# Performance work log

Hardware: AMD Instinct MI355X
Metric: run time of the kernel (lower is better)

Reference implementation:

```python
import jax, jax.numpy as jnp
import numpy as np

N_NODES = 50000
N_EDGES = 800000
H = 128
D = 128
N_LAYERS = 4
N_GRAPHS = 128
NODE_VOCAB = 32
EDGE_VOCAB = 8
BN_EPS = 1e-5


def _bn(h, g, b):
    # BatchNorm1d, training-mode statistics (biased variance), as in the torch module
    m = h.mean(axis=0)
    v = ((h - m) ** 2).mean(axis=0)
    return (h - m) * jax.lax.rsqrt(v + BN_EPS) * g + b


def _gine(x, src, dst, e, eps_l):
    # GINEConv: message = ReLU(x_src + edge_attr), sum-aggregate at dst
    msg = jax.nn.relu(x[src] + e)                      # [E, H]
    aggr = jax.ops.segment_sum(msg, dst, num_segments=N_NODES)
    return (1.0 + eps_l) * x + aggr


def _forward(x_ids, edge_index, batch, edge_attr,
             node_emb, edge_emb, eps,
             init_W1, init_b1, init_g1, init_be1, init_W2, init_b2, init_g2, init_be2,
             mp_W1, mp_g1, mp_be1, mp_W2, mp_g2, mp_be2,
             l1_W1, l1_g1, l1_b1, l1_W2, l1_g2, l1_b2,
             l2_W1, l2_g1, l2_b1, l2_W2, l2_g2, l2_b2,
             fin_W):
    src, dst = edge_index[0], edge_index[1]
    x = node_emb[x_ids]                                # [N, H]
    e = edge_emb[edge_attr]                            # [E, H]
    # initialization conv (Linear layers WITH bias)
    h = _gine(x, src, dst, e, eps[0])
    h = jax.nn.relu(_bn(h @ init_W1 + init_b1, init_g1, init_be1))
    x = jax.nn.relu(_bn(h @ init_W2 + init_b2, init_g2, init_be2))
    # message-passing layers (Linear layers WITHOUT bias)
    for i in range(N_LAYERS):
        h = _gine(x, src, dst, e, eps[1 + i])
        h = jax.nn.relu(_bn(h @ mp_W1[i], mp_g1[i], mp_be1[i]))
        x = jax.nn.relu(_bn(h @ mp_W2[i], mp_g2[i], mp_be2[i]))
    # readout: global_add_pool
    g = jax.ops.segment_sum(x, batch, num_segments=N_GRAPHS)   # [G, H]
    # lin1 (outer F.relu is idempotent; dropout = identity in eval)
    h = jax.nn.relu(_bn(g @ l1_W1, l1_g1, l1_b1))
    h = jax.nn.relu(_bn(h @ l1_W2, l1_g2, l1_b2))
    # lin2
    h = jax.nn.relu(_bn(h @ l2_W1, l2_g1, l2_b1))
    h = jax.nn.relu(_bn(h @ l2_W2, l2_g2, l2_b2))
    return h @ fin_W                                   # [G, 1]


def setup_inputs() -> dict:
    key = jax.random.key(0)
    ks = jax.random.split(key, 20)
    s = 1.0 / np.sqrt(H)
    rn = lambda k, shp, sc: jax.random.normal(k, shp, dtype=jnp.float32) * sc
    return {
        "x_ids": jax.random.randint(ks[0], (N_NODES,), 0, NODE_VOCAB),
        "edge_index": jax.random.randint(ks[1], (2, N_EDGES), 0, N_NODES),
        "batch": jnp.sort(jax.random.randint(ks[2], (N_NODES,), 0, N_GRAPHS)),
        "edge_attr": jax.random.randint(ks[14], (N_EDGES,), 0, EDGE_VOCAB),
        "node_emb": rn(ks[3], (NODE_VOCAB, H), 0.05),
        "edge_emb": rn(ks[4], (EDGE_VOCAB, H), 0.05),
        "eps": jnp.zeros((N_LAYERS + 1,), jnp.float32),
        "init_W1": rn(ks[5], (H, D), s), "init_b1": jnp.zeros((D,)),
        "init_g1": jnp.ones((D,)), "init_be1": jnp.zeros((D,)),
        "init_W2": rn(ks[6], (D, H), s), "init_b2": jnp.zeros((H,)),
        "init_g2": jnp.ones((H,)), "init_be2": jnp.zeros((H,)),
        "mp_W1": rn(ks[7], (N_LAYERS, H, D), s),
        "mp_g1": jnp.ones((N_LAYERS, D)), "mp_be1": jnp.zeros((N_LAYERS, D)),
        "mp_W2": rn(ks[8], (N_LAYERS, D, H), s),
        "mp_g2": jnp.ones((N_LAYERS, H)), "mp_be2": jnp.zeros((N_LAYERS, H)),
        "l1_W1": rn(ks[9], (H, D), s), "l1_g1": jnp.ones((D,)), "l1_b1": jnp.zeros((D,)),
        "l1_W2": rn(ks[10], (D, D), s), "l1_g2": jnp.ones((D,)), "l1_b2": jnp.zeros((D,)),
        "l2_W1": rn(ks[11], (D, D), s), "l2_g1": jnp.ones((D,)), "l2_b1": jnp.zeros((D,)),
        "l2_W2": rn(ks[12], (D, H), s), "l2_g2": jnp.ones((H,)), "l2_b2": jnp.zeros((H,)),
        "fin_W": rn(ks[13], (H, 1), s),
    }


def reference(x_ids, edge_index, batch, edge_attr,
              node_emb, edge_emb, eps,
              init_W1, init_b1, init_g1, init_be1, init_W2, init_b2, init_g2, init_be2,
              mp_W1, mp_g1, mp_be1, mp_W2, mp_g2, mp_be2,
              l1_W1, l1_g1, l1_b1, l1_W2, l1_g2, l1_b2,
              l2_W1, l2_g1, l2_b1, l2_W2, l2_g2, l2_b2,
              fin_W):
    return _forward(x_ids, edge_index, batch, edge_attr,
                    node_emb, edge_emb, eps,
                    init_W1, init_b1, init_g1, init_be1, init_W2, init_b2, init_g2, init_be2,
                    mp_W1, mp_g1, mp_be1, mp_W2, mp_g2, mp_be2,
                    l1_W1, l1_g1, l1_b1, l1_W2, l1_g2, l1_b2,
                    l2_W1, l2_g1, l2_b1, l2_W2, l2_g2, l2_b2,
                    fin_W)
```

## Files before the change

### kernel.cpp

```cpp
#include <hip/hip_runtime.h>

#define NN 50000
#define NE 800000
#define NG 128
#define HD 128
#define NL 4
#define BN_EPS 1e-5f
#define REP 32
#define WP 136
#define NB 392
#define EPB 4096

typedef __attribute__((ext_vector_type(8))) short bf16x8;
typedef __attribute__((ext_vector_type(4))) float f32x4;

__device__ __forceinline__ unsigned short f2bf(float f) {
    unsigned u = __float_as_uint(f);
    u += 0x7FFFu + ((u >> 16) & 1u);
    return (unsigned short)(u >> 16);
}
__device__ __forceinline__ float bfval(unsigned short h) { return __uint_as_float((unsigned)h << 16); }
__device__ __forceinline__ float bflo(unsigned u) { return __uint_as_float(u << 16); }
__device__ __forceinline__ float bfhi(unsigned u) { return __uint_as_float(u & 0xFFFF0000u); }

// ... 14 lines not shown
    if (gam == nullptr) { scs[t] = 1.f; shs[t] = 0.f; return; }
    float s = 0.f, q = 0.f;
#pragma unroll
    for (int r = 0; r < REP; r++) {
        s += SQbase[r * 256 + t];
        q += SQbase[r * 256 + 128 + t];
    }
    float m = s * inv_cnt;
    float var = fmaxf(fmaf(q, inv_cnt, -m * m), 0.f);
    float inv = rsqrtf(var + BN_EPS);
    float sc = gam[t] * inv;
    scs[t] = sc;
    shs[t] = fmaf(-m, sc, bet[t]);
}

__global__ __launch_bounds__(256) void setup_kernel(const int* __restrict__ ids,
                                                    const float* __restrict__ emb,
                                                    unsigned short* __restrict__ Yb,
                                                    const float* __restrict__ iw1,
                                                    const float* __restrict__ iw2,
                                                    const float* __restrict__ mw1,
                                                    const float* __restrict__ mw2,
                                                    unsigned short* __restrict__ Wh,
                                                    unsigned short* __restrict__ Wl,
                                                    const int* __restrict__ dst,
                                                    int* __restrict__ deg) {
    int b = blockIdx.x, t = threadIdx.x;
    if (b < 3125) {
        int i = b * 256 + t;
        if (i < NN * 16) {
            int node = i >> 4, g = i & 15;
            int id = ids[node];
            const float* p = emb + (size_t)id * HD + 8 * g;
            float4 a = *(const float4*)p;
            float4 bb = *(const float4*)(p + 4);
            uint4 o;
            o.x = pack2(a.x, a.y); o.y = pack2(a.z, a.w);
            o.z = pack2(bb.x, bb.y); o.w = pack2(bb.z, bb.w);
            *(uint4*)(Yb + (size_t)node * HD + 8 * g) = o;
        }
    } else if (b < 3765) {
        int i = (b - 3125) * 256 + t;
        if (i < 163840) {
            int seg = i >> 14, loc = i & 16383;
            float v;
            if (seg == 0)      v = iw1[loc];
            else if (seg == 1) v = iw2[loc];
            else if (seg < 6)  v = mw1[(seg - 2) * 16384 + loc];
            else               v = mw2[(seg - 6) * 16384 + loc];
            int k = loc >> 7, n = loc & 127;
            unsigned short h = f2bf(v);
            float r = v - bfval(h);
            Wh[seg * 16384 + n * 128 + k] = h;
            Wl[seg * 16384 + n * 128 + k] = f2bf(r);
        }
    } else {
        int e = (b - 3765) * 256 + t;
        if (e < NE) atomicAdd(&deg[dst[e]], 1);
    }
}

__global__ __launch_bounds__(256) void ybn_kernel(const float* __restrict__ X,
                                                  const float* __restrict__ SQin,
                                                  const float* __restrict__ gam,
                                                  const float* __restrict__ bet,
                                                  unsigned short* __restrict__ Yb) {
    __shared__ float scs[HD], shs[HD];
    int t = threadIdx.x;
    if (t < HD) bn_pre(SQin, gam, bet, 1.f / NN, t, scs, shs);
    __syncthreads();
    int row = blockIdx.x * 16 + (t >> 4);
    int c8 = (t & 15) * 8;
    if (row < NN) {
        const float* p = X + (size_t)row * HD + c8;
        float4 v0 = *(const float4*)p;
        float4 v1 = *(const float4*)(p + 4);
        float4 s0 = *(const float4*)&scs[c8], s1 = *(const float4*)&scs[c8 + 4];
        float4 h0 = *(const float4*)&shs[c8], h1 = *(const float4*)&shs[c8 + 4];
        float f0 = fmaxf(fmaf(v0.x, s0.x, h0.x), 0.f), f1 = fmaxf(fmaf(v0.y, s0.y, h0.y), 0.f);
        float f2 = fmaxf(fmaf(v0.z, s0.z, h0.z), 0.f), f3 = fmaxf(fmaf(v0.w, s0.w, h0.w), 0.f);
        float f4 = fmaxf(fmaf(v1.x, s1.x, h1.x), 0.f), f5 = fmaxf(fmaf(v1.y, s1.y, h1.y), 0.f);
        float f6 = fmaxf(fmaf(v1.z, s1.z, h1.z), 0.f), f7 = fmaxf(fmaf(v1.w, s1.w, h1.w), 0.f);
        uint4 o;
        o.x = pack2(f0, f1); o.y = pack2(f2, f3);
        o.z = pack2(f4, f5); o.w = pack2(f6, f7);
        *(uint4*)(Yb + (size_t)row * HD + c8) = o;
    }
}

__global__ __launch_bounds__(1024) void scan1_kernel(const int* __restrict__ deg,
                                                     int* __restrict__ rowptr,
                                                     int* __restrict__ blockSum) {
    __shared__ int s[1024];
    int b = blockIdx.x, t = threadIdx.x;
    int i = b * 1024 + t;
    int v = (i < NN) ? deg[i] : 0;
    s[t] = v;
    __syncthreads();
    for (int off = 1; off < 1024; off <<= 1) {
        int u = (t >= off) ? s[t - off] : 0;
        __syncthreads();
        s[t] += u;
        __syncthreads();
    }
    if (i < NN) rowptr[i] = s[t] - v;
    if (t == 1023) blockSum[b] = s[1023];
}

__global__ __launch_bounds__(64) void scan2_kernel(const int* __restrict__ blockSum,
                                                   int* __restrict__ blockOff,
                                                   int* __restrict__ rowptr, int nblocks) {
    int t = threadIdx.x;
    int orig = (t < nblocks) ? blockSum[t] : 0;
    int v = orig;
    for (int off = 1; off < 64; off <<= 1) {
        int u = __shfl_up(v, off, 64);
        if (t >= off) v += u;
    }
    if (t < nblocks) blockOff[t] = v - orig;
    if (t == nblocks - 1) rowptr[NN] = v;
}

__global__ __launch_bounds__(1024) void scan3_kernel(int* __restrict__ rowptr,
                                                     int* __restrict__ cursor,
                                                     const int* __restrict__ blockOff,
                                                     int* __restrict__ bucketCursor) {
    int b = blockIdx.x, t = threadIdx.x;
    int i = b * 1024 + t;
    if (i < NN) {
        int r = rowptr[i] + blockOff[b];
        rowptr[i] = r;
        cursor[i] = r;
        if ((i & 127) == 0) bucketCursor[i >> 7] = r;
    }
}

__global__ __launch_bounds__(256) void bin_kernel(const int* __restrict__ src,
                                                  const int* __restrict__ dst,
                                                  const int* __restrict__ attr,
                                                  int* __restrict__ bucketCursor,
                                                  uint2* __restrict__ ebuf) {
    __shared__ int cnt[512];
    __shared__ int sc[512], sc2[512];
    __shared__ int base[512];
    __shared__ int garr[NB];
    __shared__ int wof[NB];
    __shared__ uint2 stage[EPB];
    int t = threadIdx.x;
    int e0 = blockIdx.x * EPB;
    for (int i = t; i < 512; i += 256) cnt[i] = 0;
    __syncthreads();
    int myb[16]; unsigned myv[16]; int myd[16];
#pragma unroll
    for (int j = 0; j < 16; j++) {
        int e = e0 + t + j * 256;
        if (e < NE) {
            int d = dst[e];
            myd[j] = d;
            myv[j] = (unsigned)src[e] | ((unsigned)attr[e] << 16);
            myb[j] = d >> 7;
            atomicAdd(&cnt[myb[j]], 1);
        } else myb[j] = -1;
    }
    __syncthreads();
    for (int k = t; k < 512; k += 256) sc[k] = cnt[k];
    __syncthreads();
    int* sp = sc; int* dp = sc2;
    for (int off = 1; off < 512; off <<= 1) {
        for (int k = t; k < 512; k += 256) dp[k] = sp[k] + (k >= off ? sp[k - off] : 0);
        __syncthreads();
        int* tmp = sp; sp = dp; dp = tmp;
    }
    for (int k = t; k < 512; k += 256) base[k] = sp[k] - cnt[k];
    int total = sp[511];
    __syncthreads();
    for (int b = t; b < NB; b += 256) {
        wof[b] = 0;
        if (cnt[b] > 0) garr[b] = atomicAdd(&bucketCursor[b], cnt[b]);
    }
    __syncthreads();
#pragma unroll
    for (int j = 0; j < 16; j++) {
        if (myb[j] >= 0) {
            int slot = base[myb[j]] + atomicAdd(&wof[myb[j]], 1);
            stage[slot] = make_uint2(myv[j], (unsigned)myd[j]);
        }
    }
    __syncthreads();
    for (int i = t; i < total; i += 256) {
        uint2 u = stage[i];
        int b = (int)(u.y >> 7);
        ebuf[garr[b] + (i - base[b])] = u;
    }
}

__global__ __launch_bounds__(256) void place_kernel(const uint2* __restrict__ ebuf,
                                                    const int* __restrict__ rowptr,
                                                    int* __restrict__ cursor,
                                                    unsigned* __restrict__ csr) {
    int b = blockIdx.x;
    int n0 = b * 128;
    int n1 = n0 + 128; if (n1 > NN) n1 = NN;
    int es = rowptr[n0], ee = rowptr[n1];
    for (int i = es + threadIdx.x; i < ee; i += 256) {
        uint2 u = ebuf[i];
        int pos = atomicAdd(&cursor[u.y], 1);
        csr[pos] = u.x;
    }
}

__device__ __forceinline__ void gine_acc(const unsigned short* __restrict__ Yb,
                                         const float* __restrict__ elds,
                                         unsigned p, int cq, float mask, float* a) {
    uint4 q = *(const uint4*)(Yb + (size_t)(p & 0xFFFFu) * HD + 8 * cq);
    const float* ep = elds + (p >> 16) * HD + 8 * cq;
    float4 e0 = *(const float4*)ep;
    float4 e1 = *(const float4*)(ep + 4);
    a[0] += mask * fmaxf(bflo(q.x) + e0.x, 0.f);
    a[1] += mask * fmaxf(bfhi(q.x) + e0.y, 0.f);
    a[2] += mask * fmaxf(bflo(q.y) + e0.z, 0.f);
    a[3] += mask * fmaxf(bfhi(q.y) + e0.w, 0.f);
    a[4] += mask * fmaxf(bflo(q.z) + e1.x, 0.f);
    a[5] += mask * fmaxf(bfhi(q.z) + e1.y, 0.f);
    a[6] += mask * fmaxf(bflo(q.w) + e1.z, 0.f);
    a[7] += mask * fmaxf(bfhi(q.w) + e1.w, 0.f);
}

__global__ __launch_bounds__(256) void conv_kernel(const unsigned short* __restrict__ Yb,
                                                   const int* __restrict__ rowptr,
                                                   const unsigned* __restrict__ csr,
                                                   const float* __restrict__ edge_emb,
                                                   const float* __restrict__ eps, int layer,
                                                   unsigned short* __restrict__ Ah,
                                                   unsigned short* __restrict__ Al) {
    __shared__ float elds[8 * HD];
    int t = threadIdx.x;
    ((float4*)elds)[t] = ((const float4*)edge_emb)[t];
    __syncthreads();
    int wave = t >> 6, lane = t & 63;
    int node = blockIdx.x * 4 + wave;
    if (node >= NN) return;
    int sub = lane >> 4, cq = lane & 15;
    int lo = rowptr[node], hi = rowptr[node + 1];
    float a[8];
#pragma unroll
    for (int i = 0; i < 8; i++) a[i] = 0.f;
    for (int base = lo; base < hi; base += 64) {
        unsigned pl = 0;
        int cnt = hi - base; if (cnt > 64) cnt = 64;
        if (base + lane < hi) pl = csr[base + lane];
        int j = 0;
        for (; j + 16 <= cnt; j += 16) {
            unsigned pa = __shfl(pl, j + sub, 64);
            unsigned pb = __shfl(pl, j + 4 + sub, 64);
            unsigned pc = __shfl(pl, j + 8 + sub, 64);
            unsigned pd = __shfl(pl, j + 12 + sub, 64);
            gine_acc(Yb, elds, pa, cq, 1.f, a);
            gine_acc(Yb, elds, pb, cq, 1.f, a);
            gine_acc(Yb, elds, pc, cq, 1.f, a);
            gine_acc(Yb, elds, pd, cq, 1.f, a);
        }
        for (; j + 8 <= cnt; j += 8) {
            unsigned pa = __shfl(pl, j + sub, 64);
            unsigned pb = __shfl(pl, j + 4 + sub, 64);
            gine_acc(Yb, elds, pa, cq, 1.f, a);
            gine_acc(Yb, elds, pb, cq, 1.f, a);
        }
        for (; j < cnt; j += 4) {
            int je = j + sub;
            bool val = (je < cnt);
            unsigned p = __shfl(pl, val ? je : j, 64);
            gine_acc(Yb, elds, p, cq, val ? 1.f : 0.f, a);
        }
    }
#pragma unroll
    for (int i = 0; i < 8; i++) {
        a[i] += __shfl_xor(a[i], 16, 64);
        a[i] += __shfl_xor(a[i], 32, 64);
    }
    if (sub == 0) {
        float g = 1.f + eps[layer];
        uint4 q = *(const uint4*)(Yb + (size_t)node * HD + 8 * cq);
        float o0 = fmaf(g, bflo(q.x), a[0]), o1 = fmaf(g, bfhi(q.x), a[1]);
        float o2 = fmaf(g, bflo(q.y), a[2]), o3 = fmaf(g, bfhi(q.y), a[3]);
        float o4 = fmaf(g, bflo(q.z), a[4]), o5 = fmaf(g, bfhi(q.z), a[5]);
        float o6 = fmaf(g, bflo(q.w), a[6]), o7 = fmaf(g, bfhi(q.w), a[7]);
        uint4 H, L;
        split2(o0, o1, H.x, L.x);
        split2(o2, o3, H.y, L.y);
        split2(o4, o5, H.z, L.z);
        split2(o6, o7, H.w, L.w);
        *(uint4*)(Ah + (size_t)node * HD + 8 * cq) = H;
        *(uint4*)(Al + (size_t)node * HD + 8 * cq) = L;
    }
}

__global__ __launch_bounds__(256) void mm_mfma_pre(const unsigned short* __restrict__ Ah,
                                                   const unsigned short* __restrict__ Al,
                                                   const unsigned short* __restrict__ Wh,
                                                   const unsigned short* __restrict__ Wl,
                                                   const float* __restrict__ bias,
                                                   float* __restrict__ out,
                                                   float* __restrict__ SQout) {
    __shared__ unsigned short WhS[64 * WP];
    __shared__ unsigned short WlS[64 * WP];
    int t = threadIdx.x;
    int rowblk = blockIdx.x >> 1;
    int colbase = (blockIdx.x & 1) * 64;
    const unsigned short* sh = Wh + (size_t)colbase * HD;
    const unsigned short* sl = Wl + (size_t)colbase * HD;
#pragma unroll
    for (int i = 0; i < 4; i++) {
        int idx = t + i * 256;
        int col = idx >> 4, kk = (idx & 15) * 8;
        *(uint4*)(WhS + col * WP + kk) = *(const uint4*)(sh + (size_t)col * HD + kk);
        *(uint4*)(WlS + col * WP + kk) = *(const uint4*)(sl + (size_t)col * HD + kk);
    }
    __syncthreads();
    int w = t >> 6, lane = t & 63;
    int quad = lane >> 4, nl = lane & 15;
    int row0 = rowblk * 128 + w * 32;
    int rA0 = row0 + nl, rA1 = row0 + 16 + nl;
    bool ok0 = rA0 < NN, ok1 = rA1 < NN;
    f32x4 acc[8];
#pragma unroll
    for (int i = 0; i < 8; i++) acc[i] = (f32x4){0.f, 0.f, 0.f, 0.f};
#pragma unroll
    for (int kc = 0; kc < 4; kc++) {
        int k0 = kc * 32 + quad * 8;
        bf16x8 a0h = ok0 ? *(const bf16x8*)(Ah + (size_t)rA0 * HD + k0) : (bf16x8)0;
        bf16x8 a0l = ok0 ? *(const bf16x8*)(Al + (size_t)rA0 * HD + k0) : (bf16x8)0;
        bf16x8 a1h = ok1 ? *(const bf16x8*)(Ah + (size_t)rA1 * HD + k0) : (bf16x8)0;
        bf16x8 a1l = ok1 ? *(const bf16x8*)(Al + (size_t)rA1 * HD + k0) : (bf16x8)0;
#pragma unroll
        for (int c = 0; c < 4; c++) {
            int wof = (c * 16 + nl) * WP + k0;
            bf16x8 bh = *(const bf16x8*)(WhS + wof);
            bf16x8 bl = *(const bf16x8*)(WlS + wof);
            acc[c] = __builtin_amdgcn_mfma_f32_16x16x32_bf16(a0h, bh, acc[c], 0, 0, 0);
            acc[c] = __builtin_amdgcn_mfma_f32_16x16x32_bf16(a0l, bh, acc[c], 0, 0, 0);
            acc[c] = __builtin_amdgcn_mfma_f32_16x16x32_bf16(a0h, bl, acc[c], 0, 0, 0);
            acc[4 + c] = __builtin_amdgcn_mfma_f32_16x16x32_bf16(a1h, bh, acc[4 + c], 0, 0, 0);
            acc[4 + c] = __builtin_amdgcn_mfma_f32_16x16x32_bf16(a1l, bh, acc[4 + c], 0, 0, 0);
            acc[4 + c] = __builtin_amdgcn_mfma_f32_16x16x32_bf16(a1h, bl, acc[4 + c], 0, 0, 0);
        }
    }
    int rep = (blockIdx.x & (REP - 1)) * 256;
#pragma unroll
    for (int h = 0; h < 2; h++) {
        int baserow = row0 + h * 16 + quad * 4;
#pragma unroll
        for (int c = 0; c < 4; c++) {
            int col = colbase + c * 16 + nl;
            float bv = bias ? bias[col] : 0.f;
            f32x4 v = acc[h * 4 + c];
            float s = 0.f, qq = 0.f;
#pragma unroll
            for (int r = 0; r < 4; r++) {
                int grow = baserow + r;
                float val = v[r] + bv;
                if (grow < NN) {
                    out[(size_t)grow * HD + col] = val;
                    s += val;
                    qq += val * val;
                }
            }
            s += __shfl_xor(s, 16, 64);  s += __shfl_xor(s, 32, 64);
            qq += __shfl_xor(qq, 16, 64); qq += __shfl_xor(qq, 32, 64);
            if (quad == 0) {
                atomicAdd(&SQout[rep + col], s);
                atomicAdd(&SQout[rep + 128 + col], qq);
            }
        }
    }
}

__global__ __launch_bounds__(256) void mm_mfma_act(const float* __restrict__ A,
                                                   const unsigned short* __restrict__ Wh,
                                                   const unsigned short* __restrict__ Wl,
                                                   const float* __restrict__ bias,
                                                   const float* __restrict__ SQin,
                                                   const float* __restrict__ gam,
                                                   const float* __restrict__ bet,
                                                   float* __restrict__ out,
                                                   float* __restrict__ SQout) {
    __shared__ unsigned short WhS[64 * WP];
    __shared__ unsigned short WlS[64 * WP];
    __shared__ float scs[HD], shs[HD];
    int t = threadIdx.x;
    int rowblk = blockIdx.x >> 1;
    int colbase = (blockIdx.x & 1) * 64;
    if (t < HD) bn_pre(SQin, gam, bet, 1.f / NN, t, scs, shs);
    const unsigned short* sh = Wh + (size_t)colbase * HD;
    const unsigned short* sl = Wl + (size_t)colbase * HD;
#pragma unroll
    for (int i = 0; i < 4; i++) {
        int idx = t + i * 256;
        int col = idx >> 4, kk = (idx & 15) * 8;
        *(uint4*)(WhS + col * WP + kk) = *(const uint4*)(sh + (size_t)col * HD + kk);
        *(uint4*)(WlS + col * WP + kk) = *(const uint4*)(sl + (size_t)col * HD + kk);
    }
    __syncthreads();
    int w = t >> 6, lane = t & 63;
    int quad = lane >> 4, nl = lane & 15;
    int row0 = rowblk * 128 + w * 32;
    int rA0 = row0 + nl, rA1 = row0 + 16 + nl;
    bool ok0 = rA0 < NN, ok1 = rA1 < NN;
    f32x4 acc[8];
#pragma unroll
    for (int i = 0; i < 8; i++) acc[i] = (f32x4){0.f, 0.f, 0.f, 0.f};
#pragma unroll
    for (int kc = 0; kc < 4; kc++) {
        int k0 = kc * 32 + quad * 8;
        float4 s0 = *(const float4*)&scs[k0], s1 = *(const float4*)&scs[k0 + 4];
        float4 t0 = *(const float4*)&shs[k0], t1 = *(const float4*)&shs[k0 + 4];
        bf16x8 a0h, a0l, a1h, a1l;
        {
            float4 v0 = ok0 ? *(const float4*)(A + (size_t)rA0 * HD + k0) : make_float4(0, 0, 0, 0);
            float4 v1 = ok0 ? *(const float4*)(A + (size_t)rA0 * HD + k0 + 4) : make_float4(0, 0, 0, 0);
            float f0 = fmaxf(fmaf(v0.x, s0.x, t0.x), 0.f), f1 = fmaxf(fmaf(v0.y, s0.y, t0.y), 0.f);
            float f2 = fmaxf(fmaf(v0.z, s0.z, t0.z), 0.f), f3 = fmaxf(fmaf(v0.w, s0.w, t0.w), 0.f);
            float f4 = fmaxf(fmaf(v1.x, s1.x, t1.x), 0.f), f5 = fmaxf(fmaf(v1.y, s1.y, t1.y), 0.f);
            float f6 = fmaxf(fmaf(v1.z, s1.z, t1.z), 0.f), f7 = fmaxf(fmaf(v1.w, s1.w, t1.w), 0.f);
            if (!ok0) { f0 = f1 = f2 = f3 = f4 = f5 = f6 = f7 = 0.f; }
            unsigned h0, h1, h2, h3, l0, l1, l2, l3;
            split2(f0, f1, h0, l0); split2(f2, f3, h1, l1);
            split2(f4, f5, h2, l2); split2(f6, f7, h3, l3);
            a0h = __builtin_bit_cast(bf16x8, make_uint4(h0, h1, h2, h3));
            a0l = __builtin_bit_cast(bf16x8, make_uint4(l0, l1, l2, l3));
        }
        {
            float4 v0 = ok1 ? *(const float4*)(A + (size_t)rA1 * HD + k0) : make_float4(0, 0, 0, 0);
            float4 v1 = ok1 ? *(const float4*)(A + (size_t)rA1 * HD + k0 + 4) : make_float4(0, 0, 0, 0);
            float f0 = fmaxf(fmaf(v0.x, s0.x, t0.x), 0.f), f1 = fmaxf(fmaf(v0.y, s0.y, t0.y), 0.f);
            float f2 = fmaxf(fmaf(v0.z, s0.z, t0.z), 0.f), f3 = fmaxf(fmaf(v0.w, s0.w, t0.w), 0.f);
            float f4 = fmaxf(fmaf(v1.x, s1.x, t1.x), 0.f), f5 = fmaxf(fmaf(v1.y, s1.y, t1.y), 0.f);
            float f6 = fmaxf(fmaf(v1.z, s1.z, t1.z), 0.f), f7 = fmaxf(fmaf(v1.w, s1.w, t1.w), 0.f);
            if (!ok1) { f0 = f1 = f2 = f3 = f4 = f5 = f6 = f7 = 0.f; }
            unsigned h0, h1, h2, h3, l0, l1, l2, l3;
            split2(f0, f1, h0, l0); split2(f2, f3, h1, l1);
            split2(f4, f5, h2, l2); split2(f6, f7, h3, l3);
            a1h = __builtin_bit_cast(bf16x8, make_uint4(h0, h1, h2, h3));
            a1l = __builtin_bit_cast(bf16x8, make_uint4(l0, l1, l2, l3));
        }
#pragma unroll
        for (int c = 0; c < 4; c++) {
            int wof = (c * 16 + nl) * WP + k0;
            bf16x8 bh = *(const bf16x8*)(WhS + wof);
            bf16x8 bl = *(const bf16x8*)(WlS + wof);
            acc[c] = __builtin_amdgcn_mfma_f32_16x16x32_bf16(a0h, bh, acc[c], 0, 0, 0);
            acc[c] = __builtin_amdgcn_mfma_f32_16x16x32_bf16(a0l, bh, acc[c], 0, 0, 0);
            acc[c] = __builtin_amdgcn_mfma_f32_16x16x32_bf16(a0h, bl, acc[c], 0, 0, 0);
            acc[4 + c] = __builtin_amdgcn_mfma_f32_16x16x32_bf16(a1h, bh, acc[4 + c], 0, 0, 0);
            acc[4 + c] = __builtin_amdgcn_mfma_f32_16x16x32_bf16(a1l, bh, acc[4 + c], 0, 0, 0);
            acc[4 + c] = __builtin_amdgcn_mfma_f32_16x16x32_bf16(a1h, bl, acc[4 + c], 0, 0, 0);
        }
    }
    int rep = (blockIdx.x & (REP - 1)) * 256;
#pragma unroll
    for (int h = 0; h < 2; h++) {
        int baserow = row0 + h * 16 + quad * 4;
#pragma unroll
        for (int c = 0; c < 4; c++) {
            int col = colbase + c * 16 + nl;
            float bv = bias ? bias[col] : 0.f;
            f32x4 v = acc[h * 4 + c];
            float s = 0.f, qq = 0.f;
#pragma unroll
            for (int r = 0; r < 4; r++) {
                int grow = baserow + r;
                float val = v[r] + bv;
                if (grow < NN) {
                    out[(size_t)grow * HD + col] = val;
                    s += val;
                    qq += val * val;
                }
            }
            s += __shfl_xor(s, 16, 64);  s += __shfl_xor(s, 32, 64);
            qq += __shfl_xor(qq, 16, 64); qq += __shfl_xor(qq, 32, 64);
            if (quad == 0) {
                atomicAdd(&SQout[rep + col], s);
                atomicAdd(&SQout[rep + 128 + col], qq);
            }
        }
    }
}

__global__ __launch_bounds__(256) void readout_kernel(const float* __restrict__ x,
                                                      const int* __restrict__ batch,
                                                      const float* __restrict__ SQin,
                                                      const float* __restrict__ gam,
                                                      const float* __restrict__ bet,
                                                      float* __restrict__ gout) {
    __shared__ int bat[256];
    __shared__ float scs[HD], shs[HD];
    int t = threadIdx.x;
    int rq = t >> 5, cq = t & 31;
    int r0 = blockIdx.x * 256;
    int i = r0 + t;
    bat[t] = (i < NN) ? batch[i] : -1;
    if (t < HD) bn_pre(SQin, gam, bet, 1.f / NN, t, scs, shs);
    __syncthreads();
    float4 s4 = *(const float4*)&scs[4 * cq];
    float4 h4 = *(const float4*)&shs[4 * cq];
    float4 acc = make_float4(0.f, 0.f, 0.f, 0.f);
    int gcur = -1;
    for (int j = rq; j < 256; j += 8) {
        int r = r0 + j;
        if (r >= NN) break;
        int g = bat[j];
        if (g != gcur) {
            if (gcur >= 0) {
                atomicAdd(&gout[(size_t)gcur * HD + 4 * cq + 0], acc.x);
                atomicAdd(&gout[(size_t)gcur * HD + 4 * cq + 1], acc.y);
                atomicAdd(&gout[(size_t)gcur * HD + 4 * cq + 2], acc.z);
                atomicAdd(&gout[(size_t)gcur * HD + 4 * cq + 3], acc.w);
            }
            acc = make_float4(0.f, 0.f, 0.f, 0.f);
            gcur = g;
        }
        float4 v = *(const float4*)(x + (size_t)r * HD + 4 * cq);
        acc.x += fmaxf(fmaf(v.x, s4.x, h4.x), 0.f);
        acc.y += fmaxf(fmaf(v.y, s4.y, h4.y), 0.f);
        acc.z += fmaxf(fmaf(v.z, s4.z, h4.z), 0.f);
        acc.w += fmaxf(fmaf(v.w, s4.w, h4.w), 0.f);
    }
    if (gcur >= 0) {
        atomicAdd(&gout[(size_t)gcur * HD + 4 * cq + 0], acc.x);
        atomicAdd(&gout[(size_t)gcur * HD + 4 * cq + 1], acc.y);
        atomicAdd(&gout[(size_t)gcur * HD + 4 * cq + 2], acc.z);
        atomicAdd(&gout[(size_t)gcur * HD + 4 * cq + 3], acc.w);
    }
}

__global__ __launch_bounds__(256) void head_mm(const float* __restrict__ A,
                                               const float* __restrict__ W,
                                               const float* __restrict__ SQin,
                                               const float* __restrict__ gam,
                                               const float* __restrict__ bet,
                                               float* __restrict__ out,
                                               float* __restrict__ SQout) {
    const int PADK = 132;
    __shared__ float As[64 * PADK];
    __shared__ float colS[HD], colQ[HD];
    __shared__ float scs[HD], shs[HD];
    int t = threadIdx.x;
    if (t < HD) {
        colS[t] = 0.f; colQ[t] = 0.f;
        bn_pre(SQin, gam, bet, 1.f / NG, t, scs, shs);
    }
    __syncthreads();
    int row0 = blockIdx.x * 64;
#pragma unroll
    for (int i = 0; i < 8; i++) {
        int idx = t + i * 256;
        int r = idx >> 5, kq = idx & 31;
        float4 v = *(const float4*)(A + (size_t)(row0 + r) * HD + 4 * kq);
        float4 s4 = *(const float4*)&scs[4 * kq];
        float4 h4 = *(const float4*)&shs[4 * kq];
        v.x = fmaxf(fmaf(v.x, s4.x, h4.x), 0.f);
        v.y = fmaxf(fmaf(v.y, s4.y, h4.y), 0.f);
        v.z = fmaxf(fmaf(v.z, s4.z, h4.z), 0.f);
        v.w = fmaxf(fmaf(v.w, s4.w, h4.w), 0.f);
        *(float4*)&As[r * PADK + 4 * kq] = v;
    }
    __syncthreads();
    int jq = t & 31, rb = t >> 5;
    float acc[8][4];
#pragma unroll
    for (int i = 0; i < 8; i++)
#pragma unroll
        for (int j = 0; j < 4; j++) acc[i][j] = 0.f;
    const float* Wp = W + 4 * jq;
    const float* Ap = &As[rb * 8 * PADK];
    for (int k = 0; k < HD; k += 4) {
        float4 w0 = *(const float4*)(Wp + (size_t)(k + 0) * HD);
        float4 w1 = *(const float4*)(Wp + (size_t)(k + 1) * HD);
        float4 w2 = *(const float4*)(Wp + (size_t)(k + 2) * HD);
        float4 w3 = *(const float4*)(Wp + (size_t)(k + 3) * HD);
#pragma unroll
        for (int i = 0; i < 8; i++) {
            float4 a4 = *(const float4*)&Ap[i * PADK + k];
            acc[i][0] = fmaf(a4.x, w0.x, acc[i][0]);
            acc[i][1] = fmaf(a4.x, w0.y, acc[i][1]);
            acc[i][2] = fmaf(a4.x, w0.z, acc[i][2]);
            acc[i][3] = fmaf(a4.x, w0.w, acc[i][3]);
            acc[i][0] = fmaf(a4.y, w1.x, acc[i][0]);
            acc[i][1] = fmaf(a4.y, w1.y, acc[i][1]);
            acc[i][2] = fmaf(a4.y, w1.z, acc[i][2]);
            acc[i][3] = fmaf(a4.y, w1.w, acc[i][3]);
            acc[i][0] = fmaf(a4.z, w2.x, acc[i][0]);
            acc[i][1] = fmaf(a4.z, w2.y, acc[i][1]);
            acc[i][2] = fmaf(a4.z, w2.z, acc[i][2]);
            acc[i][3] = fmaf(a4.z, w2.w, acc[i][3]);
            acc[i][0] = fmaf(a4.w, w3.x, acc[i][0]);
            acc[i][1] = fmaf(a4.w, w3.y, acc[i][1]);
            acc[i][2] = fmaf(a4.w, w3.z, acc[i][2]);
            acc[i][3] = fmaf(a4.w, w3.w, acc[i][3]);
        }
    }
    float s0 = 0, s1 = 0, s2 = 0, s3 = 0, q0 = 0, q1 = 0, q2 = 0, q3 = 0;
#pragma unroll
    for (int i = 0; i < 8; i++) {
        int gr = row0 + rb * 8 + i;
        float4 v = make_float4(acc[i][0], acc[i][1], acc[i][2], acc[i][3]);
        *(float4*)(out + (size_t)gr * HD + 4 * jq) = v;
        s0 += v.x; q0 += v.x * v.x;
        s1 += v.y; q1 += v.y * v.y;
        s2 += v.z; q2 += v.z * v.z;
        s3 += v.w; q3 += v.w * v.w;
    }
    atomicAdd(&colS[4 * jq + 0], s0); atomicAdd(&colQ[4 * jq + 0], q0);
    atomicAdd(&colS[4 * jq + 1], s1); atomicAdd(&colQ[4 * jq + 1], q1);
    atomicAdd(&colS[4 * jq + 2], s2); atomicAdd(&colQ[4 * jq + 2], q2);
    atomicAdd(&colS[4 * jq + 3], s3); atomicAdd(&colQ[4 * jq + 3], q3);
    __syncthreads();
    int rep = (blockIdx.x & (REP - 1)) * 256;
    if (t < HD) {
        atomicAdd(&SQout[rep + t], colS[t]);
        atomicAdd(&SQout[rep + 128 + t], colQ[t]);
    }
}

__global__ __launch_bounds__(128) void final_kernel(const float* __restrict__ h,
                                                    const float* __restrict__ SQin,
                                                    const float* __restrict__ gam,
                                                    const float* __restrict__ bet,
                                                    const float* __restrict__ finW,
                                                    float* __restrict__ out) {
    __shared__ float scs[HD], shs[HD];
    int t = threadIdx.x;
    bn_pre(SQin, gam, bet, 1.f / NG, t, scs, shs);
    __syncthreads();
    float s = 0.f;
    for (int c = 0; c < HD; c++) {
        float v = h[(size_t)t * HD + c];
        v = fmaxf(fmaf(v, scs[c], shs[c]), 0.f);
        s += v * finW[c];
    }
    out[t] = s;
}

extern "C" void kernel_launch(void* const* d_in, const int* in_sizes, int n_in,
                              void* d_out, int out_size, void* d_ws, size_t ws_size,
                              hipStream_t stream) {
    const int* x_ids = (const int*)d_in[0];
    const int* edge_index = (const int*)d_in[1];
    const int* batch = (const int*)d_in[2];
    const int* edge_attr = (const int*)d_in[3];
    const float* node_emb = (const float*)d_in[4];
    const float* edge_emb = (const float*)d_in[5];
    const float* eps = (const float*)d_in[6];
    const float* init_W1 = (const float*)d_in[7];
    const float* init_b1 = (const float*)d_in[8];
    const float* init_g1 = (const float*)d_in[9];
    const float* init_be1 = (const float*)d_in[10];
    const float* init_W2 = (const float*)d_in[11];
    const float* init_b2 = (const float*)d_in[12];
    const float* init_g2 = (const float*)d_in[13];
    const float* init_be2 = (const float*)d_in[14];
    const float* mp_W1 = (const float*)d_in[15];
    const float* mp_g1 = (const float*)d_in[16];
    const float* mp_be1 = (const float*)d_in[17];
    const float* mp_W2 = (const float*)d_in[18];
    const float* mp_g2 = (const float*)d_in[19];
    const float* mp_be2 = (const float*)d_in[20];
    const float* l1_W1 = (const float*)d_in[21];
    const float* l1_g1 = (const float*)d_in[22];
    const float* l1_b1 = (const float*)d_in[23];
    const float* l1_W2 = (const float*)d_in[24];
    const float* l1_g2 = (const float*)d_in[25];
    const float* l1_b2 = (const float*)d_in[26];
    const float* l2_W1 = (const float*)d_in[27];
    const float* l2_g1 = (const float*)d_in[28];
    const float* l2_b1 = (const float*)d_in[29];
    const float* l2_W2 = (const float*)d_in[30];
    const float* l2_g2 = (const float*)d_in[31];
    const float* l2_b2 = (const float*)d_in[32];
    const float* fin_W = (const float*)d_in[33];

    const int* e_src = edge_index;
    const int* e_dst = edge_index + NE;

    const size_t STG = (size_t)REP * 256;
    float* ws = (float*)d_ws;
    float* X = ws;
    float* Bbuf = X + (size_t)NN * HD;
    unsigned short* Yb = (unsigned short*)Bbuf;
    unsigned short* Ah = (unsigned short*)(Bbuf + (size_t)NN * HD);
    unsigned short* Al = Ah + (size_t)NN * HD;
    float* SQ = (float*)(Al + (size_t)NN * HD);
    float* Gp = SQ + 14 * STG;
    int* deg = (int*)(Gp + NG * HD);
    float* Hp = (float*)(deg + 50048);
    float* Hp2 = Hp + NG * HD;
    int* rowptr = (int*)(Hp2 + NG * HD);
    int* cursor = rowptr + 50048;
    int* blockSum = cursor + 50048;
    int* blockOff = blockSum + 64;
    int* bucketCursor = blockOff + 64;
    unsigned* csr = (unsigned*)(bucketCursor + NB);
    unsigned short* Wh = (unsigned short*)(csr + NE);
    unsigned short* Wl = Wh + 163840;
    uint2* ebuf = (uint2*)(Wl + 163840);

    const size_t zero_bytes = (14 * STG + NG * HD) * sizeof(float) + 50048 * sizeof(int);
    hipMemsetAsync(SQ, 0, zero_bytes, stream);

    const int SCAN_BLOCKS = (NN + 1023) / 1024;
    setup_kernel<<<6890, 256, 0, stream>>>(x_ids, node_emb, Yb, init_W1, init_W2, mp_W1,
                                           mp_W2, Wh, Wl, e_dst, deg);
    scan1_kernel<<<SCAN_BLOCKS, 1024, 0, stream>>>(deg, rowptr, blockSum);
    scan2_kernel<<<1, 64, 0, stream>>>(blockSum, blockOff, rowptr, SCAN_BLOCKS);
    scan3_kernel<<<SCAN_BLOCKS, 1024, 0, stream>>>(rowptr, cursor, blockOff, bucketCursor);
    bin_kernel<<<(NE + EPB - 1) / EPB, 256, 0, stream>>>(e_src, e_dst, edge_attr,
                                                         bucketCursor, ebuf);
    place_kernel<<<(NN + 127) / 128, 256, 0, stream>>>(ebuf, rowptr, cursor, csr);

    const int mfma_grid = ((NN + 127) / 128) * 2;
    const int ybn_grid = (NN + 15) / 16;
    for (int i = 0; i <= NL; i++) {
        const unsigned short* Wh1 = Wh + (size_t)(i == 0 ? 0 : 2 + (i - 1)) * 16384;
        const unsigned short* Wl1 = Wl + (size_t)(i == 0 ? 0 : 2 + (i - 1)) * 16384;
        const unsigned short* Wh2 = Wh + (size_t)(i == 0 ? 1 : 6 + (i - 1)) * 16384;
        const unsigned short* Wl2 = Wl + (size_t)(i == 0 ? 1 : 6 + (i - 1)) * 16384;
        const float* b1 = (i == 0) ? init_b1 : nullptr;
        const float* b2 = (i == 0) ? init_b2 : nullptr;
        const float* g1 = (i == 0) ? init_g1 : mp_g1 + (size_t)(i - 1) * HD;
        const float* be1 = (i == 0) ? init_be1 : mp_be1 + (size_t)(i - 1) * HD;
        const float* gp = (i == 1) ? init_g2 : mp_g2 + (size_t)(i - 2) * HD;
        const float* bp = (i == 1) ? init_be2 : mp_be2 + (size_t)(i - 2) * HD;
        float* Sprev = SQ + (size_t)(2 * i - 1) * STG;
        float* S1 = SQ + (size_t)(2 * i) * STG;
        float* S2 = SQ + (size_t)(2 * i + 1) * STG;

        if (i > 0) ybn_kernel<<<ybn_grid, 256, 0, stream>>>(X, Sprev, gp, bp, Yb);
        conv_kernel<<<(NN + 3) / 4, 256, 0, stream>>>(Yb, rowptr, csr, edge_emb, eps, i, Ah, Al);
        mm_mfma_pre<<<mfma_grid, 256, 0, stream>>>(Ah, Al, Wh1, Wl1, b1, Bbuf, S1);
        mm_mfma_act<<<mfma_grid, 256, 0, stream>>>(Bbuf, Wh2, Wl2, b2, S1, g1, be1, X, S2);
    }

    float* S9 = SQ + 9 * STG;
    readout_kernel<<<(NN + 255) / 256, 256, 0, stream>>>(
        X, batch, S9, mp_g2 + 3 * HD, mp_be2 + 3 * HD, Gp);

    float* S10 = SQ + 10 * STG;
    float* S11 = SQ + 11 * STG;
    float* S12 = SQ + 12 * STG;
    float* S13 = SQ + 13 * STG;
    head_mm<<<2, 256, 0, stream>>>(Gp, l1_W1, nullptr, nullptr, nullptr, Hp, S10);
    head_mm<<<2, 256, 0, stream>>>(Hp, l1_W2, S10, l1_g1, l1_b1, Hp2, S11);
    head_mm<<<2, 256, 0, stream>>>(Hp2, l2_W1, S11, l1_g2, l1_b2, Hp, S12);
    head_mm<<<2, 256, 0, stream>>>(Hp, l2_W2, S12, l2_g1, l2_b1, Hp2, S13);
    final_kernel<<<1, 128, 0, stream>>>(Hp2, S13, l2_g2, l2_b2, fin_W, (float*)d_out);
}
```

Measured before the change: 772.1 us.

## Widen MFMA tiles to full 128 columns and fuse head MLP into one kernel

```diff
diff --git a/kernel.cpp b/kernel.cpp
--- a/kernel.cpp
+++ b/kernel.cpp
@@ -340,19 +340,16 @@
                                                    const float* __restrict__ bias,
                                                    float* __restrict__ out,
                                                    float* __restrict__ SQout) {
-    __shared__ unsigned short WhS[64 * WP];
-    __shared__ unsigned short WlS[64 * WP];
+    __shared__ unsigned short WhS[128 * WP];
+    __shared__ unsigned short WlS[128 * WP];
     int t = threadIdx.x;
-    int rowblk = blockIdx.x >> 1;
-    int colbase = (blockIdx.x & 1) * 64;
-    const unsigned short* sh = Wh + (size_t)colbase * HD;
-    const unsigned short* sl = Wl + (size_t)colbase * HD;
-#pragma unroll
-    for (int i = 0; i < 4; i++) {
+    int rowblk = blockIdx.x;
+#pragma unroll
+    for (int i = 0; i < 8; i++) {
         int idx = t + i * 256;
         int col = idx >> 4, kk = (idx & 15) * 8;
-        *(uint4*)(WhS + col * WP + kk) = *(const uint4*)(sh + (size_t)col * HD + kk);
-        *(uint4*)(WlS + col * WP + kk) = *(const uint4*)(sl + (size_t)col * HD + kk);
+        *(uint4*)(WhS + col * WP + kk) = *(const uint4*)(Wh + (size_t)col * HD + kk);
+        *(uint4*)(WlS + col * WP + kk) = *(const uint4*)(Wl + (size_t)col * HD + kk);
     }
     __syncthreads();
     int w = t >> 6, lane = t & 63;
@@ -360,9 +357,9 @@
     int row0 = rowblk * 128 + w * 32;
     int rA0 = row0 + nl, rA1 = row0 + 16 + nl;
     bool ok0 = rA0 < NN, ok1 = rA1 < NN;
-    f32x4 acc[8];
-#pragma unroll
-    for (int i = 0; i < 8; i++) acc[i] = (f32x4){0.f, 0.f, 0.f, 0.f};
+    f32x4 acc[16];
+#pragma unroll
+    for (int i = 0; i < 16; i++) acc[i] = (f32x4){0.f, 0.f, 0.f, 0.f};
 #pragma unroll
     for (int kc = 0; kc < 4; kc++) {
         int k0 = kc * 32 + quad * 8;
@@ -371,16 +368,16 @@
         bf16x8 a1h = ok1 ? *(const bf16x8*)(Ah + (size_t)rA1 * HD + k0) : (bf16x8)0;
         bf16x8 a1l = ok1 ? *(const bf16x8*)(Al + (size_t)rA1 * HD + k0) : (bf16x8)0;
 #pragma unroll
-        for (int c = 0; c < 4; c++) {
+        for (int c = 0; c < 8; c++) {
             int wof = (c * 16 + nl) * WP + k0;
             bf16x8 bh = *(const bf16x8*)(WhS + wof);
             bf16x8 bl = *(const bf16x8*)(WlS + wof);
             acc[c] = __builtin_amdgcn_mfma_f32_16x16x32_bf16(a0h, bh, acc[c], 0, 0, 0);
             acc[c] = __builtin_amdgcn_mfma_f32_16x16x32_bf16(a0l, bh, acc[c], 0, 0, 0);
             acc[c] = __builtin_amdgcn_mfma_f32_16x16x32_bf16(a0h, bl, acc[c], 0, 0, 0);
-            acc[4 + c] = __builtin_amdgcn_mfma_f32_16x16x32_bf16(a1h, bh, acc[4 + c], 0, 0, 0);
-            acc[4 + c] = __builtin_amdgcn_mfma_f32_16x16x32_bf16(a1l, bh, acc[4 + c], 0, 0, 0);
-            acc[4 + c] = __builtin_amdgcn_mfma_f32_16x16x32_bf16(a1h, bl, acc[4 + c], 0, 0, 0);
+            acc[8 + c] = __builtin_amdgcn_mfma_f32_16x16x32_bf16(a1h, bh, acc[8 + c], 0, 0, 0);
+            acc[8 + c] = __builtin_amdgcn_mfma_f32_16x16x32_bf16(a1l, bh, acc[8 + c], 0, 0, 0);
+            acc[8 + c] = __builtin_amdgcn_mfma_f32_16x16x32_bf16(a1h, bl, acc[8 + c], 0, 0, 0);
         }
     }
     int rep = (blockIdx.x & (REP - 1)) * 256;
@@ -388,10 +385,10 @@
     for (int h = 0; h < 2; h++) {
         int baserow = row0 + h * 16 + quad * 4;
 #pragma unroll
-        for (int c = 0; c < 4; c++) {
-            int col = colbase + c * 16 + nl;
+        for (int c = 0; c < 8; c++) {
+            int col = c * 16 + nl;
             float bv = bias ? bias[col] : 0.f;
-            f32x4 v = acc[h * 4 + c];
+            f32x4 v = acc[h * 8 + c];
             float s = 0.f, qq = 0.f;
 #pragma unroll
             for (int r = 0; r < 4; r++) {
@@ -422,21 +419,18 @@
                                                    const float* __restrict__ bet,
                                                    float* __restrict__ out,
                                                    float* __restrict__ SQout) {
-    __shared__ unsigned short WhS[64 * WP];
-    __shared__ unsigned short WlS[64 * WP];
+    __shared__ unsigned short WhS[128 * WP];
+    __shared__ unsigned short WlS[128 * WP];
     __shared__ float scs[HD], shs[HD];
     int t = threadIdx.x;
-    int rowblk = blockIdx.x >> 1;
-    int colbase = (blockIdx.x & 1) * 64;
+    int rowblk = blockIdx.x;
     if (t < HD) bn_pre(SQin, gam, bet, 1.f / NN, t, scs, shs);
-    const unsigned short* sh = Wh + (size_t)colbase * HD;
-    const unsigned short* sl = Wl + (size_t)colbase * HD;
-#pragma unroll
-    for (int i = 0; i < 4; i++) {
+#pragma unroll
+    for (int i = 0; i < 8; i++) {
         int idx = t + i * 256;
         int col = idx >> 4, kk = (idx & 15) * 8;
-        *(uint4*)(WhS + col * WP + kk) = *(const uint4*)(sh + (size_t)col * HD + kk);
-        *(uint4*)(WlS + col * WP + kk) = *(const uint4*)(sl + (size_t)col * HD + kk);
+        *(uint4*)(WhS + col * WP + kk) = *(const uint4*)(Wh + (size_t)col * HD + kk);
+        *(uint4*)(WlS + col * WP + kk) = *(const uint4*)(Wl + (size_t)col * HD + kk);
     }
     __syncthreads();
     int w = t >> 6, lane = t & 63;
@@ -444,9 +438,9 @@
     int row0 = rowblk * 128 + w * 32;
     int rA0 = row0 + nl, rA1 = row0 + 16 + nl;
     bool ok0 = rA0 < NN, ok1 = rA1 < NN;
-    f32x4 acc[8];
-#pragma unroll
-    for (int i = 0; i < 8; i++) acc[i] = (f32x4){0.f, 0.f, 0.f, 0.f};
+    f32x4 acc[16];
+#pragma unroll
+    for (int i = 0; i < 16; i++) acc[i] = (f32x4){0.f, 0.f, 0.f, 0.f};
 #pragma unroll
     for (int kc = 0; kc < 4; kc++) {
         int k0 = kc * 32 + quad * 8;
@@ -482,16 +476,16 @@
             a1l = __builtin_bit_cast(bf16x8, make_uint4(l0, l1, l2, l3));
         }
 #pragma unroll
-        for (int c = 0; c < 4; c++) {
+        for (int c = 0; c < 8; c++) {
             int wof = (c * 16 + nl) * WP + k0;
             bf16x8 bh = *(const bf16x8*)(WhS + wof);
             bf16x8 bl = *(const bf16x8*)(WlS + wof);
             acc[c] = __builtin_amdgcn_mfma_f32_16x16x32_bf16(a0h, bh, acc[c], 0, 0, 0);
             acc[c] = __builtin_amdgcn_mfma_f32_16x16x32_bf16(a0l, bh, acc[c], 0, 0, 0);
             acc[c] = __builtin_amdgcn_mfma_f32_16x16x32_bf16(a0h, bl, acc[c], 0, 0, 0);
-            acc[4 + c] = __builtin_amdgcn_mfma_f32_16x16x32_bf16(a1h, bh, acc[4 + c], 0, 0, 0);
-            acc[4 + c] = __builtin_amdgcn_mfma_f32_16x16x32_bf16(a1l, bh, acc[4 + c], 0, 0, 0);
-            acc[4 + c] = __builtin_amdgcn_mfma_f32_16x16x32_bf16(a1h, bl, acc[4 + c], 0, 0, 0);
+            acc[8 + c] = __builtin_amdgcn_mfma_f32_16x16x32_bf16(a1h, bh, acc[8 + c], 0, 0, 0);
+            acc[8 + c] = __builtin_amdgcn_mfma_f32_16x16x32_bf16(a1l, bh, acc[8 + c], 0, 0, 0);
+            acc[8 + c] = __builtin_amdgcn_mfma_f32_16x16x32_bf16(a1h, bl, acc[8 + c], 0, 0, 0);
         }
     }
     int rep = (blockIdx.x & (REP - 1)) * 256;
@@ -499,10 +493,10 @@
     for (int h = 0; h < 2; h++) {
         int baserow = row0 + h * 16 + quad * 4;
 #pragma unroll
-        for (int c = 0; c < 4; c++) {
-            int col = colbase + c * 16 + nl;
+        for (int c = 0; c < 8; c++) {
+            int col = c * 16 + nl;
             float bv = bias ? bias[col] : 0.f;
-            f32x4 v = acc[h * 4 + c];
+            f32x4 v = acc[h * 8 + c];
             float s = 0.f, qq = 0.f;
 #pragma unroll
             for (int r = 0; r < 4; r++) {
@@ -571,112 +565,147 @@
     }
 }
 
-__global__ __launch_bounds__(256) void head_mm(const float* __restrict__ A,
-                                               const float* __restrict__ W,
-                                               const float* __restrict__ SQin,
-                                               const float* __restrict__ gam,
-                                               const float* __restrict__ bet,
-                                               float* __restrict__ out,
-                                               float* __restrict__ SQout) {
-    const int PADK = 132;
-    __shared__ float As[64 * PADK];
-    __shared__ float colS[HD], colQ[HD];
-    __shared__ float scs[HD], shs[HD];
+__global__ __launch_bounds__(256) void head_fused(const float* __restrict__ Gp,
+                                                  const float* __restrict__ Wa,
+                                                  const float* __restrict__ Wb,
+                                                  const float* __restrict__ Wc,
+                                                  const float* __restrict__ Wd,
+                                                  const float* __restrict__ g0,
+                                                  const float* __restrict__ b0,
+                                                  const float* __restrict__ g1,
+                                                  const float* __restrict__ b1,
+                                                  const float* __restrict__ g2,
+                                                  const float* __restrict__ b2,
+                                                  const float* __restrict__ g3,
+                                                  const float* __restrict__ b3,
+                                                  const float* __restrict__ finW,
+                                                  float* __restrict__ out) {
+    const int AP = 132;
+    __shared__ float A_lds[128 * AP];
+    __shared__ unsigned short WhS[128 * WP];
+    __shared__ unsigned short WlS[128 * WP];
+    __shared__ float colS[HD], colQ[HD], scs[HD], shs[HD];
     int t = threadIdx.x;
+    if (t < HD) { colS[t] = 0.f; colQ[t] = 0.f; scs[t] = 1.f; shs[t] = 0.f; }
+#pragma unroll
+    for (int i = 0; i < 16; i++) {
+        int idx = t + i * 256;
+        int r = idx >> 5, cq = (idx & 31) * 4;
+        *(float4*)&A_lds[r * AP + cq] = *(const float4*)(Gp + (size_t)r * HD + cq);
+    }
+    int w = t >> 6, lane = t & 63;
+    int quad = lane >> 4, nl = lane & 15;
+    int row0 = w * 32;
+    const float* Ws[4] = {Wa, Wb, Wc, Wd};
+    const float* Gs[4] = {g0, g1, g2, g3};
+    const float* Bs[4] = {b0, b1, b2, b3};
+    for (int s = 0; s < 4; s++) {
+        const float* W = Ws[s];
+        for (int i = t; i < 4096; i += 256) {
+            int k = i >> 5, n = (i & 31) * 4;
+            float4 v = *(const float4*)(W + (size_t)k * HD + n);
+            unsigned short h0 = f2bf(v.x), h1 = f2bf(v.y), h2 = f2bf(v.z), h3 = f2bf(v.w);
+            WhS[(n + 0) * WP + k] = h0; WlS[(n + 0) * WP + k] = f2bf(v.x - bfval(h0));
+            WhS[(n + 1) * WP + k] = h1; WlS[(n + 1) * WP + k] = f2bf(v.y - bfval(h1));
+            WhS[(n + 2) * WP + k] = h2; WlS[(n + 2) * WP + k] = f2bf(v.z - bfval(h2));
+            WhS[(n + 3) * WP + k] = h3; WlS[(n + 3) * WP + k] = f2bf(v.w - bfval(h3));
+        }
+        __syncthreads();
+        f32x4 acc[16];
+#pragma unroll
+        for (int i = 0; i < 16; i++) acc[i] = (f32x4){0.f, 0.f, 0.f, 0.f};
+#pragma unroll
+        for (int kc = 0; kc < 4; kc++) {
+            int k0 = kc * 32 + quad * 8;
+            float4 s0 = *(const float4*)&scs[k0], s1 = *(const float4*)&scs[k0 + 4];
+            float4 t0 = *(const float4*)&shs[k0], t1 = *(const float4*)&shs[k0 + 4];
+            bf16x8 a0h, a0l, a1h, a1l;
+            {
+                const float* ap = &A_lds[(row0 + nl) * AP + k0];
+                float4 v0 = *(const float4*)ap;
+                float4 v1 = *(const float4*)(ap + 4);
+                float f0 = fmaxf(fmaf(v0.x, s0.x, t0.x), 0.f), f1 = fmaxf(fmaf(v0.y, s0.y, t0.y), 0.f);
+                float f2 = fmaxf(fmaf(v0.z, s0.z, t0.z), 0.f), f3 = fmaxf(fmaf(v0.w, s0.w, t0.w), 0.f);
+                float f4 = fmaxf(fmaf(v1.x, s1.x, t1.x), 0.f), f5 = fmaxf(fmaf(v1.y, s1.y, t1.y), 0.f);
+                float f6 = fmaxf(fmaf(v1.z, s1.z, t1.z), 0.f), f7 = fmaxf(fmaf(v1.w, s1.w, t1.w), 0.f);
+                unsigned h0, h1, h2, h3, l0, l1, l2, l3;
+                split2(f0, f1, h0, l0); split2(f2, f3, h1, l1);
+                split2(f4, f5, h2, l2); split2(f6, f7, h3, l3);
+                a0h = __builtin_bit_cast(bf16x8, make_uint4(h0, h1, h2, h3));
+                a0l = __builtin_bit_cast(bf16x8, make_uint4(l0, l1, l2, l3));
+            }
+            {
+                const float* ap = &A_lds[(row0 + 16 + nl) * AP + k0];
+                float4 v0 = *(const float4*)ap;
+                float4 v1 = *(const float4*)(ap + 4);
+                float f0 = fmaxf(fmaf(v0.x, s0.x, t0.x), 0.f), f1 = fmaxf(fmaf(v0.y, s0.y, t0.y), 0.f);
+                float f2 = fmaxf(fmaf(v0.z, s0.z, t0.z), 0.f), f3 = fmaxf(fmaf(v0.w, s0.w, t0.w), 0.f);
+                float f4 = fmaxf(fmaf(v1.x, s1.x, t1.x), 0.f), f5 = fmaxf(fmaf(v1.y, s1.y, t1.y), 0.f);
+                float f6 = fmaxf(fmaf(v1.z, s1.z, t1.z), 0.f), f7 = fmaxf(fmaf(v1.w, s1.w, t1.w), 0.f);
+                unsigned h0, h1, h2, h3, l0, l1, l2, l3;
+                split2(f0, f1, h0, l0); split2(f2, f3, h1, l1);
+                split2(f4, f5, h2, l2); split2(f6, f7, h3, l3);
+                a1h = __builtin_bit_cast(bf16x8, make_uint4(h0, h1, h2, h3));
+                a1l = __builtin_bit_cast(bf16x8, make_uint4(l0, l1, l2, l3));
+            }
+#pragma unroll
+            for (int c = 0; c < 8; c++) {
+                int wof = (c * 16 + nl) * WP + k0;
+                bf16x8 bh = *(const bf16x8*)(WhS + wof);
+                bf16x8 bl = *(const bf16x8*)(WlS + wof);
+                acc[c] = __builtin_amdgcn_mfma_f32_16x16x32_bf16(a0h, bh, acc[c], 0, 0, 0);
+                acc[c] = __builtin_amdgcn_mfma_f32_16x16x32_bf16(a0l, bh, acc[c], 0, 0, 0);
+                acc[c] = __builtin_amdgcn_mfma_f32_16x16x32_bf16(a0h, bl, acc[c], 0, 0, 0);
+                acc[8 + c] = __builtin_amdgcn_mfma_f32_16x16x32_bf16(a1h, bh, acc[8 + c], 0, 0, 0);
+                acc[8 + c] = __builtin_amdgcn_mfma_f32_16x16x32_bf16(a1l, bh, acc[8 + c], 0, 0, 0);
+                acc[8 + c] = __builtin_amdgcn_mfma_f32_16x16x32_bf16(a1h, bl, acc[8 + c], 0, 0, 0);
+            }
+        }
+        __syncthreads();
+#pragma unroll
+        for (int h = 0; h < 2; h++) {
+            int baserow = row0 + h * 16 + quad * 4;
+#pragma unroll
+            for (int c = 0; c < 8; c++) {
+                int col = c * 16 + nl;
+                f32x4 v = acc[h * 8 + c];
+                float ss = 0.f, qq = 0.f;
+#pragma unroll
+                for (int r = 0; r < 4; r++) {
+                    float val = v[r];
+                    A_lds[(baserow + r) * AP + col] = val;
+                    ss += val;
+                    qq += val * val;
+                }
+                ss += __shfl_xor(ss, 16, 64);  ss += __shfl_xor(ss, 32, 64);
+                qq += __shfl_xor(qq, 16, 64);  qq += __shfl_xor(qq, 32, 64);
+                if (quad == 0) {
+                    atomicAdd(&colS[col], ss);
+                    atomicAdd(&colQ[col], qq);
+                }
+            }
+        }
+        __syncthreads();
+        if (t < HD) {
+            float m = colS[t] * (1.f / NG);
+            float var = fmaxf(fmaf(colQ[t], 1.f / NG, -m * m), 0.f);
+            float inv = rsqrtf(var + BN_EPS);
+            float sc = Gs[s][t] * inv;
+            scs[t] = sc;
+            shs[t] = fmaf(-m, sc, Bs[s][t]);
+            colS[t] = 0.f;
+            colQ[t] = 0.f;
+        }
+        __syncthreads();
+    }
     if (t < HD) {
-        colS[t] = 0.f; colQ[t] = 0.f;
-        bn_pre(SQin, gam, bet, 1.f / NG, t, scs, shs);
-    }
-    __syncthreads();
-    int row0 = blockIdx.x * 64;
-#pragma unroll
-    for (int i = 0; i < 8; i++) {
-        int idx = t + i * 256;
-        int r = idx >> 5, kq = idx & 31;
-        float4 v = *(const float4*)(A + (size_t)(row0 + r) * HD + 4 * kq);
-        float4 s4 = *(const float4*)&scs[4 * kq];
-        float4 h4 = *(const float4*)&shs[4 * kq];
-        v.x = fmaxf(fmaf(v.x, s4.x, h4.x), 0.f);
-        v.y = fmaxf(fmaf(v.y, s4.y, h4.y), 0.f);
-        v.z = fmaxf(fmaf(v.z, s4.z, h4.z), 0.f);
-        v.w = fmaxf(fmaf(v.w, s4.w, h4.w), 0.f);
-        *(float4*)&As[r * PADK + 4 * kq] = v;
-    }
-    __syncthreads();
-    int jq = t & 31, rb = t >> 5;
-    float acc[8][4];
-#pragma unroll
-    for (int i = 0; i < 8; i++)
-#pragma unroll
-        for (int j = 0; j < 4; j++) acc[i][j] = 0.f;
-    const float* Wp = W + 4 * jq;
-    const float* Ap = &As[rb * 8 * PADK];
-    for (int k = 0; k < HD; k += 4) {
-        float4 w0 = *(const float4*)(Wp + (size_t)(k + 0) * HD);
-        float4 w1 = *(const float4*)(Wp + (size_t)(k + 1) * HD);
-        float4 w2 = *(const float4*)(Wp + (size_t)(k + 2) * HD);
-        float4 w3 = *(const float4*)(Wp + (size_t)(k + 3) * HD);
-#pragma unroll
-        for (int i = 0; i < 8; i++) {
-            float4 a4 = *(const float4*)&Ap[i * PADK + k];
-            acc[i][0] = fmaf(a4.x, w0.x, acc[i][0]);
-            acc[i][1] = fmaf(a4.x, w0.y, acc[i][1]);
-            acc[i][2] = fmaf(a4.x, w0.z, acc[i][2]);
-            acc[i][3] = fmaf(a4.x, w0.w, acc[i][3]);
-            acc[i][0] = fmaf(a4.y, w1.x, acc[i][0]);
-            acc[i][1] = fmaf(a4.y, w1.y, acc[i][1]);
-            acc[i][2] = fmaf(a4.y, w1.z, acc[i][2]);
-            acc[i][3] = fmaf(a4.y, w1.w, acc[i][3]);
-            acc[i][0] = fmaf(a4.z, w2.x, acc[i][0]);
-            acc[i][1] = fmaf(a4.z, w2.y, acc[i][1]);
-            acc[i][2] = fmaf(a4.z, w2.z, acc[i][2]);
-            acc[i][3] = fmaf(a4.z, w2.w, acc[i][3]);
-            acc[i][0] = fmaf(a4.w, w3.x, acc[i][0]);
-            acc[i][1] = fmaf(a4.w, w3.y, acc[i][1]);
-            acc[i][2] = fmaf(a4.w, w3.z, acc[i][2]);
-            acc[i][3] = fmaf(a4.w, w3.w, acc[i][3]);
-        }
-    }
-    float s0 = 0, s1 = 0, s2 = 0, s3 = 0, q0 = 0, q1 = 0, q2 = 0, q3 = 0;
-#pragma unroll
-    for (int i = 0; i < 8; i++) {
-        int gr = row0 + rb * 8 + i;
-        float4 v = make_float4(acc[i][0], acc[i][1], acc[i][2], acc[i][3]);
-        *(float4*)(out + (size_t)gr * HD + 4 * jq) = v;
-        s0 += v.x; q0 += v.x * v.x;
-        s1 += v.y; q1 += v.y * v.y;
-        s2 += v.z; q2 += v.z * v.z;
-        s3 += v.w; q3 += v.w * v.w;
-    }
-    atomicAdd(&colS[4 * jq + 0], s0); atomicAdd(&colQ[4 * jq + 0], q0);
-    atomicAdd(&colS[4 * jq + 1], s1); atomicAdd(&colQ[4 * jq + 1], q1);
-    atomicAdd(&colS[4 * jq + 2], s2); atomicAdd(&colQ[4 * jq + 2], q2);
-    atomicAdd(&colS[4 * jq + 3], s3); atomicAdd(&colQ[4 * jq + 3], q3);
-    __syncthreads();
-    int rep = (blockIdx.x & (REP - 1)) * 256;
-    if (t < HD) {
-        atomicAdd(&SQout[rep + t], colS[t]);
-        atomicAdd(&SQout[rep + 128 + t], colQ[t]);
-    }
-}
-
-__global__ __launch_bounds__(128) void final_kernel(const float* __restrict__ h,
-                                                    const float* __restrict__ SQin,
-                                                    const float* __restrict__ gam,
-                                                    const float* __restrict__ bet,
-                                                    const float* __restrict__ finW,
-                                                    float* __restrict__ out) {
-    __shared__ float scs[HD], shs[HD];
-    int t = threadIdx.x;
-    bn_pre(SQin, gam, bet, 1.f / NG, t, scs, shs);
-    __syncthreads();
-    float s = 0.f;
-    for (int c = 0; c < HD; c++) {
-        float v = h[(size_t)t * HD + c];
-        v = fmaxf(fmaf(v, scs[c], shs[c]), 0.f);
-        s += v * finW[c];
-    }
-    out[t] = s;
+        float ssum = 0.f;
+        for (int c = 0; c < HD; c++) {
+            float v = fmaxf(fmaf(A_lds[t * AP + c], scs[c], shs[c]), 0.f);
+            ssum += v * finW[c];
+        }
+        out[t] = ssum;
+    }
 }
 
 extern "C" void kernel_launch(void* const* d_in, const int* in_sizes, int n_in,
@@ -741,6 +770,7 @@
     unsigned short* Wh = (unsigned short*)(csr + NE);
     unsigned short* Wl = Wh + 163840;
     uint2* ebuf = (uint2*)(Wl + 163840);
+    (void)Hp; (void)Hp2;
 
     const size_t zero_bytes = (14 * STG + NG * HD) * sizeof(float) + 50048 * sizeof(int);
     hipMemsetAsync(SQ, 0, zero_bytes, stream);
@@ -755,7 +785,7 @@
                                                          bucketCursor, ebuf);
     place_kernel<<<(NN + 127) / 128, 256, 0, stream>>>(ebuf, rowptr, cursor, csr);
 
-    const int mfma_grid = ((NN + 127) / 128) * 2;
+    const int mfma_grid = (NN + 127) / 128;
     const int ybn_grid = (NN + 15) / 16;
     for (int i = 0; i <= NL; i++) {
         const unsigned short* Wh1 = Wh + (size_t)(i == 0 ? 0 : 2 + (i - 1)) * 16384;
@@ -782,13 +812,8 @@
     readout_kernel<<<(NN + 255) / 256, 256, 0, stream>>>(
         X, batch, S9, mp_g2 + 3 * HD, mp_be2 + 3 * HD, Gp);
 
-    float* S10 = SQ + 10 * STG;
-    float* S11 = SQ + 11 * STG;
-    float* S12 = SQ + 12 * STG;
-    float* S13 = SQ + 13 * STG;
-    head_mm<<<2, 256, 0, stream>>>(Gp, l1_W1, nullptr, nullptr, nullptr, Hp, S10);
-    head_mm<<<2, 256, 0, stream>>>(Hp, l1_W2, S10, l1_g1, l1_b1, Hp2, S11);
-    head_mm<<<2, 256, 0, stream>>>(Hp2, l2_W1, S11, l1_g2, l1_b2, Hp, S12);
-    head_mm<<<2, 256, 0, stream>>>(Hp, l2_W2, S12, l2_g1, l2_b1, Hp2, S13);
-    final_kernel<<<1, 128, 0, stream>>>(Hp2, S13, l2_g2, l2_b2, fin_W, (float*)d_out);
-}
+    head_fused<<<1, 256, 0, stream>>>(Gp, l1_W1, l1_W2, l2_W1, l2_W2,
+                                      l1_g1, l1_b1, l1_g2, l1_b2,
+                                      l2_g1, l2_b1, l2_g2, l2_b2,
+                                      fin_W, (float*)d_out);
+}
```

Result: slower. 791.3 us (+2.5%).
